# Optimization experiments

Measured on AMD Instinct MI355X. Metric: run time of the kernel, lower is better.

## Reference

```python
import jax, jax.numpy as jnp
import numpy as np

N_NODES = 100000
N_EDGES = 3200000
D_FEAT = 256
FILTERS = 256


def setup_inputs() -> dict:
    key = jax.random.key(0)
    k1, k2, k3, k4, k5 = jax.random.split(key, 5)
    x = jax.random.normal(k1, (N_NODES, D_FEAT), dtype=jnp.float32)
    edge_row = jax.random.randint(k2, (N_EDGES,), 0, N_NODES, dtype=jnp.int32)
    edge_col = jax.random.randint(k3, (N_EDGES,), 0, N_NODES, dtype=jnp.int32)
    edge_vals = jnp.ones((N_EDGES,), dtype=jnp.float32)
    w = jax.random.normal(k4, (D_FEAT, FILTERS), dtype=jnp.float32) * (2.0 / D_FEAT) ** 0.5  # he_normal
    b = jax.random.normal(k5, (FILTERS,), dtype=jnp.float32) * 0.05
    return {"x": x, "edge_row": edge_row, "edge_col": edge_col,
            "edge_vals": edge_vals, "w": w, "b": b}


def reference(x, edge_row, edge_col, edge_vals, w, b):
    n = x.shape[0]
    # normalize_A: D = rowsum(A); L = D^{-1/2} A D^{-1/2}
    deg = jax.ops.segment_sum(edge_vals, edge_row, num_segments=n)
    dinv = jnp.where(deg > 0, deg ** -0.5, 0.0)  # [N]
    norm_vals = edge_vals * dinv[edge_row] * dinv[edge_col]  # [E]
    # dense projection then sparse aggregation + bias + relu
    h = x @ w  # [N, F]
    msg = norm_vals[:, None] * h[edge_col]  # [E, F] gather + scale
    agg = jax.ops.segment_sum(msg, edge_row, num_segments=n)  # [N, F]
    return jax.nn.relu(agg + b)
```

## Files before the change

### kernel.cpp

```cpp
#include <hip/hip_runtime.h>
#include <hip/hip_bf16.h>


#define DF 256

typedef __attribute__((ext_vector_type(8))) short short8;
typedef __attribute__((ext_vector_type(4))) float f32x4;

__device__ __forceinline__ unsigned short f2bf(float f) {
    unsigned int u = __float_as_uint(f);
    unsigned int r = (u + 0x7fffu + ((u >> 16) & 1u)) >> 16;
    return (unsigned short)r;
}
__device__ __forceinline__ unsigned int pack2(float a, float b) {
    return (unsigned)f2bf(a) | ((unsigned)f2bf(b) << 16);
}
__device__ __forceinline__ float bflo(unsigned int u) { return __uint_as_float(u << 16); }
__device__ __forceinline__ float bfhi(unsigned int u) { return __uint_as_float(u & 0xffff0000u); }

__global__ void hist_rank_kernel(const int* __restrict__ row, int* __restrict__ cnt,
                                 int* __restrict__ rank, int E) {
    int e = blockIdx.x * blockDim.x + threadIdx.x;
    if (e < E) rank[e] = atomicAdd(&cnt[row[e]], 1);
}

__global__ __launch_bounds__(256) void scan1_kernel(const int* __restrict__ cnt,
                                                    int* __restrict__ bsum, int N) {
    __shared__ int red[256];
    int t = threadIdx.x;
    int base = blockIdx.x * 1024 + t * 4;
    int s = 0;
    if (base + 3 < N) {
        int4 v = *(const int4*)(cnt + base);
        s = v.x + v.y + v.z + v.w;
    } else {
        for (int k = 0; k < 4; ++k) if (base + k < N) s += cnt[base + k];
    }
    red[t] = s;
    __syncthreads();
    for (int off = 128; off > 0; off >>= 1) {
        if (t < off) red[t] += red[t + off];
        __syncthreads();
    }
    if (t == 0) bsum[blockIdx.x] = red[0];
}

__global__ __launch_bounds__(256) void scan2_kernel(const int* __restrict__ bsum,
                                                    int* __restrict__ bpre,
                                                    int* __restrict__ row_start, int B, int N) {
    __shared__ int ps[256];
    int t = threadIdx.x;
    int v = (t < B) ? bsum[t] : 0;
    ps[t] = v;
    __syncthreads();
    for (int off = 1; off < 256; off <<= 1) {
        int u = (t >= off) ? ps[t - off] : 0;
        __syncthreads();
        ps[t] += u;
        __syncthreads();
    }
    if (t < B) bpre[t] = ps[t] - v;
    if (t == 255) row_start[N] = ps[255];
}

__global__ __launch_bounds__(256) void scan3_kernel(const int* __restrict__ cnt,
                                                    const int* __restrict__ bpre,
                                                    int* __restrict__ row_start, int N) {
    __shared__ int ps[256];
    int t = threadIdx.x;
    int base = blockIdx.x * 1024 + t * 4;
    int v0 = 0, v1 = 0, v2 = 0, v3 = 0;
    if (base + 3 < N) {
        int4 v = *(const int4*)(cnt + base);
        v0 = v.x; v1 = v.y; v2 = v.z; v3 = v.w;
    } else {
        if (base < N) v0 = cnt[base];
        if (base + 1 < N) v1 = cnt[base + 1];
        if (base + 2 < N) v2 = cnt[base + 2];
        if (base + 3 < N) v3 = cnt[base + 3];
    }
    int tsum = v0 + v1 + v2 + v3;
    ps[t] = tsum;
    __syncthreads();
    for (int off = 1; off < 256; off <<= 1) {
        int u = (t >= off) ? ps[t - off] : 0;
        __syncthreads();
        ps[t] += u;
        __syncthreads();
    }
    int pre = bpre[blockIdx.x] + ps[t] - tsum;
    if (base < N) row_start[base] = pre;
    if (base + 1 < N) row_start[base + 1] = pre + v0;
    if (base + 2 < N) row_start[base + 2] = pre + v0 + v1;
    if (base + 3 < N) row_start[base + 3] = pre + v0 + v1 + v2;
}

__global__ void scatter_kernel(const int* __restrict__ row, const int* __restrict__ col,
                               const float* __restrict__ vals, const int* __restrict__ row_start,
                               const int* __restrict__ rank, int2* __restrict__ scv, int E) {
    int e = blockIdx.x * blockDim.x + threadIdx.x;
    if (e < E) {
        int r = row[e];
        int p = row_start[r] + rank[e];
        scv[p] = make_int2(col[e], __float_as_int(vals[e]));
    }
}

__global__ void degsum_kernel(const int2* __restrict__ scv, const int* __restrict__ row_start,
                              float* __restrict__ dinv, int N) {
    int r = blockIdx.x * blockDim.x + threadIdx.x;
    if (r < N) {
        int s = row_start[r], e = row_start[r + 1];
        float d = 0.f;
        for (int i = s; i < e; ++i) d += __int_as_float(scv[i].y);
        dinv[r] = (d > 0.f) ? (1.0f / sqrtf(d)) : 0.f;
    }
}

__global__ __launch_bounds__(256) void transpose_kernel(const float* __restrict__ w,
                                                        float* __restrict__ wT) {
    __shared__ float tile[32][33];
    int bx = blockIdx.x * 32, by = blockIdx.y * 32;
    int tx = threadIdx.x, ty = threadIdx.y;
    for (int j = ty; j < 32; j += 8) tile[j][tx] = w[(by + j) * DF + bx + tx];
    __syncthreads();
    for (int j = ty; j < 32; j += 8) wT[(bx + j) * DF + by + tx] = tile[tx][j];
}

__global__ __launch_bounds__(256) void gemm_kernel(const float* __restrict__ x,
                                                   const float* __restrict__ wT,
                                                   const float* __restrict__ dinv,
                                                   unsigned short* __restrict__ h, int N) {
    __shared__ unsigned short Al[128 * 32];
    __shared__ unsigned short Bl[128 * 32];
    int tid = threadIdx.x;
    int by = blockIdx.x, bx = blockIdx.y;
    int wv = tid >> 6, lane = tid & 63;
    int wr = wv >> 1, wc = wv & 1;
    int q = lane >> 4, mi = lane & 15;

    f32x4 acc[4][4];
#pragma unroll
    for (int i = 0; i < 4; ++i)
#pragma unroll
        for (int j = 0; j < 4; ++j) acc[i][j] = (f32x4){0.f, 0.f, 0.f, 0.f};

    int srow = tid >> 1;
    int sseg = (tid & 1) * 16;
    int axrow = by * 128 + srow; if (axrow >= N) axrow = N - 1;
    const float* ax = x + (long)axrow * DF + sseg;
    const float* bxp = wT + (long)(bx * 128 + srow) * DF + sseg;
    unsigned short* Aw = &Al[srow * 32 + sseg];
    unsigned short* Bw = &Bl[srow * 32 + sseg];

    for (int kk = 0; kk < DF; kk += 32) {
        float4 a0 = *(const float4*)(ax + kk);
        float4 a1 = *(const float4*)(ax + kk + 4);
        float4 a2 = *(const float4*)(ax + kk + 8);
        float4 a3 = *(const float4*)(ax + kk + 12);
        float4 b0 = *(const float4*)(bxp + kk);
        float4 b1 = *(const float4*)(bxp + kk + 4);
        float4 b2 = *(const float4*)(bxp + kk + 8);
        float4 b3 = *(const float4*)(bxp + kk + 12);
        __syncthreads();
        uint4 pa, pb;
        pa.x = pack2(a0.x, a0.y); pa.y = pack2(a0.z, a0.w);
        pa.z = pack2(a1.x, a1.y); pa.w = pack2(a1.z, a1.w);
        *(uint4*)Aw = pa;
        pa.x = pack2(a2.x, a2.y); pa.y = pack2(a2.z, a2.w);
        pa.z = pack2(a3.x, a3.y); pa.w = pack2(a3.z, a3.w);
        *(uint4*)(Aw + 8) = pa;
        pb.x = pack2(b0.x, b0.y); pb.y = pack2(b0.z, b0.w);
        pb.z = pack2(b1.x, b1.y); pb.w = pack2(b1.z, b1.w);
        *(uint4*)Bw = pb;
        pb.x = pack2(b2.x, b2.y); pb.y = pack2(b2.z, b2.w);
        pb.z = pack2(b3.x, b3.y); pb.w = pack2(b3.z, b3.w);
        *(uint4*)(Bw + 8) = pb;
        __syncthreads();

        short8 af[4], bf[4];
#pragma unroll
        for (int i = 0; i < 4; ++i)
            af[i] = *(const short8*)&Al[(wr * 64 + i * 16 + mi) * 32 + q * 8];
#pragma unroll
        for (int j = 0; j < 4; ++j)
            bf[j] = *(const short8*)&Bl[(wc * 64 + j * 16 + mi) * 32 + q * 8];
#pragma unroll
        for (int i = 0; i < 4; ++i)
#pragma unroll
            for (int j = 0; j < 4; ++j)
                acc[i][j] = __builtin_amdgcn_mfma_f32_16x16x32_bf16(af[i], bf[j], acc[i][j], 0, 0, 0);
    }

#pragma unroll
    for (int i = 0; i < 4; ++i) {
        int base_row = by * 128 + wr * 64 + i * 16 + q * 4;
#pragma unroll
        for (int r = 0; r < 4; ++r) {
            int rg = base_row + r;
            if (rg < N) {
                float dv = dinv[rg];
#pragma unroll
                for (int j = 0; j < 4; ++j) {
                    int cg = bx * 128 + wc * 64 + j * 16 + mi;
                    h[(long)rg * DF + cg] = f2bf(dv * acc[i][j][r]);
                }
            }
        }
    }
}

__global__ __launch_bounds__(256) void agg_kernel(const unsigned short* __restrict__ h,
                                                  const int* __restrict__ row_start,
                                                  const int2* __restrict__ scv,
                                                  const float* __restrict__ dinv,
                                                  const float* __restrict__ bias,
                                                  float* __restrict__ out, int N) {
    int wave = threadIdx.x >> 6;
    int lane = threadIdx.x & 63;
    int r = blockIdx.x * 4 + wave;
    if (r >= N) return;
    int half = lane >> 5;
    int fl = (lane & 31) * 8;
    int s = row_start[r], e = row_start[r + 1];
    float a0 = 0, a1 = 0, a2 = 0, a3 = 0, a4 = 0, a5 = 0, a6 = 0, a7 = 0;
    const unsigned short* hp = h + fl;
    int i = s + half;
    for (; i + 6 < e; i += 8) {
        int2 e0 = scv[i], e1 = scv[i + 2], e2 = scv[i + 4], e3 = scv[i + 6];
        uint4 u0 = *(const uint4*)(hp + (long)e0.x * DF);
        uint4 u1 = *(const uint4*)(hp + (long)e1.x * DF);
        uint4 u2 = *(const uint4*)(hp + (long)e2.x * DF);
        uint4 u3 = *(const uint4*)(hp + (long)e3.x * DF);
        float v0 = __int_as_float(e0.y), v1 = __int_as_float(e1.y);
        float v2 = __int_as_float(e2.y), v3 = __int_as_float(e3.y);
        a0 += v0 * bflo(u0.x) + v1 * bflo(u1.x) + v2 * bflo(u2.x) + v3 * bflo(u3.x);
        a1 += v0 * bfhi(u0.x) + v1 * bfhi(u1.x) + v2 * bfhi(u2.x) + v3 * bfhi(u3.x);
        a2 += v0 * bflo(u0.y) + v1 * bflo(u1.y) + v2 * bflo(u2.y) + v3 * bflo(u3.y);
        a3 += v0 * bfhi(u0.y) + v1 * bfhi(u1.y) + v2 * bfhi(u2.y) + v3 * bfhi(u3.y);
        a4 += v0 * bflo(u0.z) + v1 * bflo(u1.z) + v2 * bflo(u2.z) + v3 * bflo(u3.z);
        a5 += v0 * bfhi(u0.z) + v1 * bfhi(u1.z) + v2 * bfhi(u2.z) + v3 * bfhi(u3.z);
        a6 += v0 * bflo(u0.w) + v1 * bflo(u1.w) + v2 * bflo(u2.w) + v3 * bflo(u3.w);
        a7 += v0 * bfhi(u0.w) + v1 * bfhi(u1.w) + v2 * bfhi(u2.w) + v3 * bfhi(u3.w);
    }
    for (; i < e; i += 2) {
        int2 e0 = scv[i];
        float v0 = __int_as_float(e0.y);
        uint4 u0 = *(const uint4*)(hp + (long)e0.x * DF);
        a0 += v0 * bflo(u0.x); a1 += v0 * bfhi(u0.x);
        a2 += v0 * bflo(u0.y); a3 += v0 * bfhi(u0.y);
        a4 += v0 * bflo(u0.z); a5 += v0 * bfhi(u0.z);
        a6 += v0 * bflo(u0.w); a7 += v0 * bfhi(u0.w);
    }
    a0 += __shfl_xor(a0, 32); a1 += __shfl_xor(a1, 32);
    a2 += __shfl_xor(a2, 32); a3 += __shfl_xor(a3, 32);
    a4 += __shfl_xor(a4, 32); a5 += __shfl_xor(a5, 32);
    a6 += __shfl_xor(a6, 32); a7 += __shfl_xor(a7, 32);
    if (half == 0) {
        float dr = dinv[r];
        float4 b0 = *(const float4*)(bias + fl);
        float4 b1 = *(const float4*)(bias + fl + 4);
        float4 o0, o1;
        o0.x = fmaxf(fmaf(dr, a0, b0.x), 0.f);
        o0.y = fmaxf(fmaf(dr, a1, b0.y), 0.f);
        o0.z = fmaxf(fmaf(dr, a2, b0.z), 0.f);
        o0.w = fmaxf(fmaf(dr, a3, b0.w), 0.f);
        o1.x = fmaxf(fmaf(dr, a4, b1.x), 0.f);
        o1.y = fmaxf(fmaf(dr, a5, b1.y), 0.f);
        o1.z = fmaxf(fmaf(dr, a6, b1.z), 0.f);
        o1.w = fmaxf(fmaf(dr, a7, b1.w), 0.f);
        *(float4*)(out + (long)r * DF + fl) = o0;
        *(float4*)(out + (long)r * DF + fl + 4) = o1;
    }
}

extern "C" void kernel_launch(void* const* d_in, const int* in_sizes, int n_in,
                              void* d_out, int out_size, void* d_ws, size_t ws_size,
                              hipStream_t stream) {
    const float* x   = (const float*)d_in[0];
    const int* erow  = (const int*)d_in[1];
    const int* ecol  = (const int*)d_in[2];
    const float* ev  = (const float*)d_in[3];
    const float* w   = (const float*)d_in[4];
    const float* b   = (const float*)d_in[5];
    float* out = (float*)d_out;

    int N = in_sizes[0] / DF;
    int E = in_sizes[1];

    char* ws = (char*)d_ws;
    size_t Na  = (((size_t)N * 4) + 255) & ~(size_t)255;
    size_t RSa = (((size_t)(N + 1) * 4) + 255) & ~(size_t)255;
    size_t Ea  = (((size_t)E * 4) + 255) & ~(size_t)255;

    int*   cnt    = (int*)  (ws);
    float* wT     = (float*)(ws);
    float* dinv   = (float*)(ws + Na);
    int*   rstart = (int*)  (ws + 2 * Na);
    int2*  scv    = (int2*) (ws + 2 * Na + RSa);
    char*  un     = ws + 2 * Na + RSa + 2 * Ea;
    int*   rank   = (int*)un;
    unsigned short* h = (unsigned short*)un;
    int*   bsum   = (int*)(un + 16000000);
    int*   bpre   = (int*)(un + 16000000 + 4096);

    int B1 = (N + 1023) / 1024;

    hipMemsetAsync(cnt, 0, Na, stream);

    hist_rank_kernel<<<(E + 255) / 256, 256, 0, stream>>>(erow, cnt, rank, E);
    scan1_kernel<<<B1, 256, 0, stream>>>(cnt, bsum, N);
    scan2_kernel<<<1, 256, 0, stream>>>(bsum, bpre, rstart, B1, N);
    scan3_kernel<<<B1, 256, 0, stream>>>(cnt, bpre, rstart, N);
    scatter_kernel<<<(E + 255) / 256, 256, 0, stream>>>(erow, ecol, ev, rstart, rank, scv, E);
    degsum_kernel<<<(N + 255) / 256, 256, 0, stream>>>(scv, rstart, dinv, N);
    transpose_kernel<<<dim3(8, 8), dim3(32, 8), 0, stream>>>(w, wT);
    gemm_kernel<<<dim3((N + 127) / 128, DF / 128), 256, 0, stream>>>(x, wT, dinv, h, N);
    agg_kernel<<<(N + 3) / 4, 256, 0, stream>>>(h, rstart, scv, dinv, b, out, N);
}
```

Baseline: 692.2 us.

## Privatize row histogram per XCC to use workgroup-scope atomics

The edge-row histogram now keeps eight separate count arrays, one per XCC, indexed by the hardware XCC id, and uses relaxed workgroup-scope atomics that can resolve in the local L2 instead of device-scope atomics. Each edge's rank is packed with its XCC id, the scan sums the eight copies, and it writes a per-XCC base offset that the scatter uses to place edges. This aims to cut the cost of cross-die atomics in the histogram, at the price of an eight-times-larger memset, more scan traffic and a nondeterministic edge order within each row. Correctness relies on each XCC's L2 being coherent for its own atomics, so the workgroup-scope choice is a risk.

```diff
diff --git a/kernel.cpp b/kernel.cpp
--- a/kernel.cpp
+++ b/kernel.cpp
@@ -18,23 +18,39 @@
 __device__ __forceinline__ float bflo(unsigned int u) { return __uint_as_float(u << 16); }
 __device__ __forceinline__ float bfhi(unsigned int u) { return __uint_as_float(u & 0xffff0000u); }
 
-__global__ void hist_rank_kernel(const int* __restrict__ row, int* __restrict__ cnt,
-                                 int* __restrict__ rank, int E) {
+__device__ __forceinline__ unsigned xcc_id() {
+    unsigned x;
+    asm volatile("s_getreg_b32 %0, hwreg(HW_REG_XCC_ID)" : "=s"(x));
+    return x & 7u;
+}
+
+__global__ void hist_rank_kernel(const int* __restrict__ row, int* __restrict__ cntx,
+                                 int* __restrict__ rank, int Np, int E) {
     int e = blockIdx.x * blockDim.x + threadIdx.x;
-    if (e < E) rank[e] = atomicAdd(&cnt[row[e]], 1);
-}
-
-__global__ __launch_bounds__(256) void scan1_kernel(const int* __restrict__ cnt,
-                                                    int* __restrict__ bsum, int N) {
+    if (e < E) {
+        unsigned x = xcc_id();
+        int r = row[e];
+        int lr = __hip_atomic_fetch_add(&cntx[(size_t)x * Np + r], 1,
+                                        __ATOMIC_RELAXED, __HIP_MEMORY_SCOPE_WORKGROUP);
+        rank[e] = lr | (int)(x << 27);
+    }
+}
+
+__global__ __launch_bounds__(256) void scan1_kernel(const int* __restrict__ cntx,
+                                                    int* __restrict__ bsum, int Np, int N) {
     __shared__ int red[256];
     int t = threadIdx.x;
     int base = blockIdx.x * 1024 + t * 4;
     int s = 0;
     if (base + 3 < N) {
-        int4 v = *(const int4*)(cnt + base);
-        s = v.x + v.y + v.z + v.w;
+        for (int x = 0; x < 8; ++x) {
+            int4 v = *(const int4*)(cntx + (size_t)x * Np + base);
+            s += v.x + v.y + v.z + v.w;
+        }
     } else {
-        for (int k = 0; k < 4; ++k) if (base + k < N) s += cnt[base + k];
+        for (int x = 0; x < 8; ++x)
+            for (int k = 0; k < 4; ++k)
+                if (base + k < N) s += cntx[(size_t)x * Np + base + k];
     }
     red[t] = s;
     __syncthreads();
@@ -63,23 +79,31 @@
     if (t == 255) row_start[N] = ps[255];
 }
 
-__global__ __launch_bounds__(256) void scan3_kernel(const int* __restrict__ cnt,
+__global__ __launch_bounds__(256) void scan3_kernel(const int* __restrict__ cntx,
                                                     const int* __restrict__ bpre,
-                                                    int* __restrict__ row_start, int N) {
+                                                    int* __restrict__ row_start,
+                                                    int* __restrict__ basex, int Np, int N) {
     __shared__ int ps[256];
     int t = threadIdx.x;
     int base = blockIdx.x * 1024 + t * 4;
-    int v0 = 0, v1 = 0, v2 = 0, v3 = 0;
+    int v[8][4];
     if (base + 3 < N) {
-        int4 v = *(const int4*)(cnt + base);
-        v0 = v.x; v1 = v.y; v2 = v.z; v3 = v.w;
+        for (int x = 0; x < 8; ++x) {
+            int4 q = *(const int4*)(cntx + (size_t)x * Np + base);
+            v[x][0] = q.x; v[x][1] = q.y; v[x][2] = q.z; v[x][3] = q.w;
+        }
     } else {
-        if (base < N) v0 = cnt[base];
-        if (base + 1 < N) v1 = cnt[base + 1];
-        if (base + 2 < N) v2 = cnt[base + 2];
-        if (base + 3 < N) v3 = cnt[base + 3];
-    }
-    int tsum = v0 + v1 + v2 + v3;
+        for (int x = 0; x < 8; ++x)
+            for (int k = 0; k < 4; ++k)
+                v[x][k] = (base + k < N) ? cntx[(size_t)x * Np + base + k] : 0;
+    }
+    int tot[4];
+    for (int k = 0; k < 4; ++k) {
+        int s = 0;
+        for (int x = 0; x < 8; ++x) s += v[x][k];
+        tot[k] = s;
+    }
+    int tsum = tot[0] + tot[1] + tot[2] + tot[3];
     ps[t] = tsum;
     __syncthreads();
     for (int off = 1; off < 256; off <<= 1) {
@@ -89,19 +113,38 @@
         __syncthreads();
     }
     int pre = bpre[blockIdx.x] + ps[t] - tsum;
-    if (base < N) row_start[base] = pre;
-    if (base + 1 < N) row_start[base + 1] = pre + v0;
-    if (base + 2 < N) row_start[base + 2] = pre + v0 + v1;
-    if (base + 3 < N) row_start[base + 3] = pre + v0 + v1 + v2;
+    int acc[4];
+    acc[0] = pre;
+    acc[1] = acc[0] + tot[0];
+    acc[2] = acc[1] + tot[1];
+    acc[3] = acc[2] + tot[2];
+    if (base + 3 < N) {
+        *(int4*)(row_start + base) = make_int4(acc[0], acc[1], acc[2], acc[3]);
+        for (int x = 0; x < 8; ++x) {
+            *(int4*)(basex + (size_t)x * Np + base) = make_int4(acc[0], acc[1], acc[2], acc[3]);
+            for (int k = 0; k < 4; ++k) acc[k] += v[x][k];
+        }
+    } else {
+        for (int k = 0; k < 4; ++k) if (base + k < N) row_start[base + k] = acc[k];
+        for (int x = 0; x < 8; ++x)
+            for (int k = 0; k < 4; ++k) {
+                if (base + k < N) basex[(size_t)x * Np + base + k] = acc[k];
+                acc[k] += v[x][k];
+            }
+    }
 }
 
 __global__ void scatter_kernel(const int* __restrict__ row, const int* __restrict__ col,
-                               const float* __restrict__ vals, const int* __restrict__ row_start,
-                               const int* __restrict__ rank, int2* __restrict__ scv, int E) {
+                               const float* __restrict__ vals, const int* __restrict__ basex,
+                               const int* __restrict__ rank, int2* __restrict__ scv,
+                               int Np, int E) {
     int e = blockIdx.x * blockDim.x + threadIdx.x;
     if (e < E) {
         int r = row[e];
-        int p = row_start[r] + rank[e];
+        int pk = rank[e];
+        int x = ((unsigned)pk) >> 27;
+        int lr = pk & 0x07FFFFFF;
+        int p = basex[(size_t)x * Np + r] + lr;
         scv[p] = make_int2(col[e], __float_as_int(vals[e]));
     }
 }
@@ -292,27 +335,29 @@
     size_t Na  = (((size_t)N * 4) + 255) & ~(size_t)255;
     size_t RSa = (((size_t)(N + 1) * 4) + 255) & ~(size_t)255;
     size_t Ea  = (((size_t)E * 4) + 255) & ~(size_t)255;
-
-    int*   cnt    = (int*)  (ws);
+    int Np = (int)(Na >> 2);
+
     float* wT     = (float*)(ws);
     float* dinv   = (float*)(ws + Na);
     int*   rstart = (int*)  (ws + 2 * Na);
     int2*  scv    = (int2*) (ws + 2 * Na + RSa);
+    int*   cntx   = (int*)  (ws + 2 * Na + RSa);
     char*  un     = ws + 2 * Na + RSa + 2 * Ea;
     int*   rank   = (int*)un;
     unsigned short* h = (unsigned short*)un;
     int*   bsum   = (int*)(un + 16000000);
     int*   bpre   = (int*)(un + 16000000 + 4096);
+    int*   basex  = (int*)(un + 17000000);
 
     int B1 = (N + 1023) / 1024;
 
-    hipMemsetAsync(cnt, 0, Na, stream);
-
-    hist_rank_kernel<<<(E + 255) / 256, 256, 0, stream>>>(erow, cnt, rank, E);
-    scan1_kernel<<<B1, 256, 0, stream>>>(cnt, bsum, N);
+    hipMemsetAsync(cntx, 0, 8 * Na, stream);
+
+    hist_rank_kernel<<<(E + 255) / 256, 256, 0, stream>>>(erow, cntx, rank, Np, E);
+    scan1_kernel<<<B1, 256, 0, stream>>>(cntx, bsum, Np, N);
     scan2_kernel<<<1, 256, 0, stream>>>(bsum, bpre, rstart, B1, N);
-    scan3_kernel<<<B1, 256, 0, stream>>>(cnt, bpre, rstart, N);
-    scatter_kernel<<<(E + 255) / 256, 256, 0, stream>>>(erow, ecol, ev, rstart, rank, scv, E);
+    scan3_kernel<<<B1, 256, 0, stream>>>(cntx, bpre, rstart, basex, Np, N);
+    scatter_kernel<<<(E + 255) / 256, 256, 0, stream>>>(erow, ecol, ev, basex, rank, scv, Np, E);
     degsum_kernel<<<(N + 255) / 256, 256, 0, stream>>>(scv, rstart, dinv, N);
     transpose_kernel<<<dim3(8, 8), dim3(32, 8), 0, stream>>>(w, wT);
     gemm_kernel<<<dim3((N + 127) / 128, DF / 128), 256, 0, stream>>>(x, wT, dinv, h, N);
```

Result: no change. 691.0 us (-0.2%).

## Replace per-row CSR build with bucketed radix partition and in-block row sort

Applied to the files above, without the earlier changes.

Replaces the global-atomic histogram, three-pass scan and random scatter with a coarse bucket partition: per-chunk shared-memory histograms over 128-row buckets, a column-wise scan, and a scatter using shared atomics. Degree and aggregation then work per bucket, and the aggregation kernel sorts the bucket's edges by row in LDS before doing the same gather-accumulate. This is meant to cut the cost of the global atomics and of the scattered writes during CSR construction. In exchange there are fewer, heavier aggregation blocks (one per 128 rows) with large LDS use, which lowers occupancy. Buckets larger than the LDS capacity fall back to a slow rescan of the overflow edges.

```diff
diff --git a/kernel.cpp b/kernel.cpp
--- a/kernel.cpp
+++ b/kernel.cpp
@@ -2,7 +2,11 @@
 #include <hip/hip_bf16.h>
 
 
-#define DF 256
+#define DF   256
+#define RSH  7
+#define RPB  128
+#define CAP  4800
+#define CHUNK 8192
 
 typedef __attribute__((ext_vector_type(8))) short short8;
 typedef __attribute__((ext_vector_type(4))) float f32x4;
@@ -18,102 +22,99 @@
 __device__ __forceinline__ float bflo(unsigned int u) { return __uint_as_float(u << 16); }
 __device__ __forceinline__ float bfhi(unsigned int u) { return __uint_as_float(u & 0xffff0000u); }
 
-__global__ void hist_rank_kernel(const int* __restrict__ row, int* __restrict__ cnt,
-                                 int* __restrict__ rank, int E) {
-    int e = blockIdx.x * blockDim.x + threadIdx.x;
-    if (e < E) rank[e] = atomicAdd(&cnt[row[e]], 1);
-}
-
-__global__ __launch_bounds__(256) void scan1_kernel(const int* __restrict__ cnt,
-                                                    int* __restrict__ bsum, int N) {
-    __shared__ int red[256];
+__global__ __launch_bounds__(256) void bhist_kernel(const int* __restrict__ row,
+                                                    int* __restrict__ blockhist, int NB, int E) {
+    __shared__ int hist[1024];
     int t = threadIdx.x;
-    int base = blockIdx.x * 1024 + t * 4;
-    int s = 0;
-    if (base + 3 < N) {
-        int4 v = *(const int4*)(cnt + base);
-        s = v.x + v.y + v.z + v.w;
-    } else {
-        for (int k = 0; k < 4; ++k) if (base + k < N) s += cnt[base + k];
-    }
-    red[t] = s;
-    __syncthreads();
-    for (int off = 128; off > 0; off >>= 1) {
-        if (t < off) red[t] += red[t + off];
-        __syncthreads();
-    }
-    if (t == 0) bsum[blockIdx.x] = red[0];
-}
-
-__global__ __launch_bounds__(256) void scan2_kernel(const int* __restrict__ bsum,
-                                                    int* __restrict__ bpre,
-                                                    int* __restrict__ row_start, int B, int N) {
+    for (int i = t; i < NB; i += 256) hist[i] = 0;
+    __syncthreads();
+    int base = blockIdx.x * CHUNK;
+    int end = base + CHUNK; if (end > E) end = E;
+    for (int i = base + t; i < end; i += 256)
+        atomicAdd(&hist[row[i] >> RSH], 1);
+    __syncthreads();
+    for (int i = t; i < NB; i += 256)
+        blockhist[(size_t)blockIdx.x * NB + i] = hist[i];
+}
+
+__global__ __launch_bounds__(256) void bscan_kernel(int* __restrict__ blockhist,
+                                                    int* __restrict__ buckettot, int NB, int NBLK) {
     __shared__ int ps[256];
+    int b = blockIdx.x, t = threadIdx.x;
+    int e0 = 2 * t, e1 = 2 * t + 1;
+    int v0 = (e0 < NBLK) ? blockhist[(size_t)e0 * NB + b] : 0;
+    int v1 = (e1 < NBLK) ? blockhist[(size_t)e1 * NB + b] : 0;
+    int tsum = v0 + v1;
+    ps[t] = tsum;
+    __syncthreads();
+    for (int off = 1; off < 256; off <<= 1) {
+        int v = (t >= off) ? ps[t - off] : 0;
+        __syncthreads();
+        ps[t] += v;
+        __syncthreads();
+    }
+    int pre = ps[t] - tsum;
+    if (e0 < NBLK) blockhist[(size_t)e0 * NB + b] = pre;
+    if (e1 < NBLK) blockhist[(size_t)e1 * NB + b] = pre + v0;
+    if (t == 255) buckettot[b] = ps[255];
+}
+
+__global__ __launch_bounds__(1024) void btot_kernel(const int* __restrict__ buckettot,
+                                                    int* __restrict__ bucket_base, int NB) {
+    __shared__ int ps[1024];
     int t = threadIdx.x;
-    int v = (t < B) ? bsum[t] : 0;
+    int v = (t < NB) ? buckettot[t] : 0;
     ps[t] = v;
     __syncthreads();
-    for (int off = 1; off < 256; off <<= 1) {
+    for (int off = 1; off < 1024; off <<= 1) {
         int u = (t >= off) ? ps[t - off] : 0;
         __syncthreads();
         ps[t] += u;
         __syncthreads();
     }
-    if (t < B) bpre[t] = ps[t] - v;
-    if (t == 255) row_start[N] = ps[255];
-}
-
-__global__ __launch_bounds__(256) void scan3_kernel(const int* __restrict__ cnt,
-                                                    const int* __restrict__ bpre,
-                                                    int* __restrict__ row_start, int N) {
-    __shared__ int ps[256];
-    int t = threadIdx.x;
-    int base = blockIdx.x * 1024 + t * 4;
-    int v0 = 0, v1 = 0, v2 = 0, v3 = 0;
-    if (base + 3 < N) {
-        int4 v = *(const int4*)(cnt + base);
-        v0 = v.x; v1 = v.y; v2 = v.z; v3 = v.w;
-    } else {
-        if (base < N) v0 = cnt[base];
-        if (base + 1 < N) v1 = cnt[base + 1];
-        if (base + 2 < N) v2 = cnt[base + 2];
-        if (base + 3 < N) v3 = cnt[base + 3];
-    }
-    int tsum = v0 + v1 + v2 + v3;
-    ps[t] = tsum;
-    __syncthreads();
-    for (int off = 1; off < 256; off <<= 1) {
-        int u = (t >= off) ? ps[t - off] : 0;
-        __syncthreads();
-        ps[t] += u;
-        __syncthreads();
-    }
-    int pre = bpre[blockIdx.x] + ps[t] - tsum;
-    if (base < N) row_start[base] = pre;
-    if (base + 1 < N) row_start[base + 1] = pre + v0;
-    if (base + 2 < N) row_start[base + 2] = pre + v0 + v1;
-    if (base + 3 < N) row_start[base + 3] = pre + v0 + v1 + v2;
-}
-
-__global__ void scatter_kernel(const int* __restrict__ row, const int* __restrict__ col,
-                               const float* __restrict__ vals, const int* __restrict__ row_start,
-                               const int* __restrict__ rank, int2* __restrict__ scv, int E) {
-    int e = blockIdx.x * blockDim.x + threadIdx.x;
-    if (e < E) {
-        int r = row[e];
-        int p = row_start[r] + rank[e];
-        scv[p] = make_int2(col[e], __float_as_int(vals[e]));
-    }
-}
-
-__global__ void degsum_kernel(const int2* __restrict__ scv, const int* __restrict__ row_start,
-                              float* __restrict__ dinv, int N) {
-    int r = blockIdx.x * blockDim.x + threadIdx.x;
-    if (r < N) {
-        int s = row_start[r], e = row_start[r + 1];
-        float d = 0.f;
-        for (int i = s; i < e; ++i) d += __int_as_float(scv[i].y);
-        dinv[r] = (d > 0.f) ? (1.0f / sqrtf(d)) : 0.f;
+    if (t < NB) bucket_base[t] = ps[t] - v;
+    if (t == 1023) bucket_base[NB] = ps[1023];
+}
+
+__global__ __launch_bounds__(256) void bscatter_kernel(const int* __restrict__ row,
+                                                       const int* __restrict__ col,
+                                                       const float* __restrict__ vals,
+                                                       const int* __restrict__ blockhist,
+                                                       const int* __restrict__ bucket_base,
+                                                       int2* __restrict__ bedge, int NB, int E) {
+    __shared__ int loff[1024];
+    int t = threadIdx.x, blk = blockIdx.x;
+    for (int i = t; i < NB; i += 256)
+        loff[i] = bucket_base[i] + blockhist[(size_t)blk * NB + i];
+    __syncthreads();
+    int base = blk * CHUNK;
+    int end = base + CHUNK; if (end > E) end = E;
+    for (int i = base + t; i < end; i += 256) {
+        int r = row[i];
+        int p = atomicAdd(&loff[r >> RSH], 1);
+        bedge[p] = make_int2(((r & (RPB - 1)) << 17) | col[i], __float_as_int(vals[i]));
+    }
+}
+
+__global__ __launch_bounds__(256) void deg_kernel(const int2* __restrict__ bedge,
+                                                  const int* __restrict__ bucket_base,
+                                                  float* __restrict__ dinv, int N) {
+    __shared__ float acc[RPB];
+    int b = blockIdx.x, t = threadIdx.x;
+    if (t < RPB) acc[t] = 0.f;
+    __syncthreads();
+    int s = bucket_base[b], e = bucket_base[b + 1];
+    for (int i = s + t; i < e; i += 256) {
+        int2 ed = bedge[i];
+        atomicAdd(&acc[ed.x >> 17], __int_as_float(ed.y));
+    }
+    __syncthreads();
+    if (t < RPB) {
+        int r = b * RPB + t;
+        if (r < N) {
+            float d = acc[t];
+            dinv[r] = (d > 0.f) ? (1.0f / sqrtf(d)) : 0.f;
+        }
     }
 }
 
@@ -210,67 +211,114 @@
     }
 }
 
-__global__ __launch_bounds__(256) void agg_kernel(const unsigned short* __restrict__ h,
-                                                  const int* __restrict__ row_start,
-                                                  const int2* __restrict__ scv,
-                                                  const float* __restrict__ dinv,
-                                                  const float* __restrict__ bias,
-                                                  float* __restrict__ out, int N) {
-    int wave = threadIdx.x >> 6;
-    int lane = threadIdx.x & 63;
-    int r = blockIdx.x * 4 + wave;
-    if (r >= N) return;
+__global__ __launch_bounds__(256) void aggb_kernel(const unsigned short* __restrict__ h,
+                                                   const int2* __restrict__ bedge,
+                                                   const int* __restrict__ bucket_base,
+                                                   const float* __restrict__ dinv,
+                                                   const float* __restrict__ bias,
+                                                   float* __restrict__ out, int N) {
+    __shared__ int2 ledge[CAP];
+    __shared__ int cnt[RPB];
+    __shared__ int lrs[RPB + 1];
+    __shared__ int lfill[RPB];
+    int b = blockIdx.x, t = threadIdx.x;
+    int s = bucket_base[b], e = bucket_base[b + 1];
+    int tot = e - s;
+    int cap_end = s + (tot < CAP ? tot : CAP);
+    if (t < RPB) { cnt[t] = 0; lfill[t] = 0; }
+    __syncthreads();
+    for (int i = s + t; i < cap_end; i += 256)
+        atomicAdd(&cnt[bedge[i].x >> 17], 1);
+    __syncthreads();
+    int myc = 0;
+    if (t < RPB) { myc = cnt[t]; lrs[t] = myc; }
+    __syncthreads();
+    for (int off = 1; off < RPB; off <<= 1) {
+        int v = (t < RPB && t >= off) ? lrs[t - off] : 0;
+        __syncthreads();
+        if (t < RPB) lrs[t] += v;
+        __syncthreads();
+    }
+    if (t < RPB) {
+        int iv = lrs[t];
+        lrs[t] = iv - myc;
+        if (t == RPB - 1) lrs[RPB] = iv;
+    }
+    __syncthreads();
+    for (int i = s + t; i < cap_end; i += 256) {
+        int2 ed = bedge[i];
+        int rl = ed.x >> 17;
+        int p = lrs[rl] + atomicAdd(&lfill[rl], 1);
+        ledge[p] = make_int2(ed.x & 0x1FFFF, ed.y);
+    }
+    __syncthreads();
+    int wv = t >> 6, lane = t & 63;
     int half = lane >> 5;
     int fl = (lane & 31) * 8;
-    int s = row_start[r], e = row_start[r + 1];
-    float a0 = 0, a1 = 0, a2 = 0, a3 = 0, a4 = 0, a5 = 0, a6 = 0, a7 = 0;
     const unsigned short* hp = h + fl;
-    int i = s + half;
-    for (; i + 6 < e; i += 8) {
-        int2 e0 = scv[i], e1 = scv[i + 2], e2 = scv[i + 4], e3 = scv[i + 6];
-        uint4 u0 = *(const uint4*)(hp + (long)e0.x * DF);
-        uint4 u1 = *(const uint4*)(hp + (long)e1.x * DF);
-        uint4 u2 = *(const uint4*)(hp + (long)e2.x * DF);
-        uint4 u3 = *(const uint4*)(hp + (long)e3.x * DF);
-        float v0 = __int_as_float(e0.y), v1 = __int_as_float(e1.y);
-        float v2 = __int_as_float(e2.y), v3 = __int_as_float(e3.y);
-        a0 += v0 * bflo(u0.x) + v1 * bflo(u1.x) + v2 * bflo(u2.x) + v3 * bflo(u3.x);
-        a1 += v0 * bfhi(u0.x) + v1 * bfhi(u1.x) + v2 * bfhi(u2.x) + v3 * bfhi(u3.x);
-        a2 += v0 * bflo(u0.y) + v1 * bflo(u1.y) + v2 * bflo(u2.y) + v3 * bflo(u3.y);
-        a3 += v0 * bfhi(u0.y) + v1 * bfhi(u1.y) + v2 * bfhi(u2.y) + v3 * bfhi(u3.y);
-        a4 += v0 * bflo(u0.z) + v1 * bflo(u1.z) + v2 * bflo(u2.z) + v3 * bflo(u3.z);
-        a5 += v0 * bfhi(u0.z) + v1 * bfhi(u1.z) + v2 * bfhi(u2.z) + v3 * bfhi(u3.z);
-        a6 += v0 * bflo(u0.w) + v1 * bflo(u1.w) + v2 * bflo(u2.w) + v3 * bflo(u3.w);
-        a7 += v0 * bfhi(u0.w) + v1 * bfhi(u1.w) + v2 * bfhi(u2.w) + v3 * bfhi(u3.w);
-    }
-    for (; i < e; i += 2) {
-        int2 e0 = scv[i];
-        float v0 = __int_as_float(e0.y);
-        uint4 u0 = *(const uint4*)(hp + (long)e0.x * DF);
-        a0 += v0 * bflo(u0.x); a1 += v0 * bfhi(u0.x);
-        a2 += v0 * bflo(u0.y); a3 += v0 * bfhi(u0.y);
-        a4 += v0 * bflo(u0.z); a5 += v0 * bfhi(u0.z);
-        a6 += v0 * bflo(u0.w); a7 += v0 * bfhi(u0.w);
-    }
-    a0 += __shfl_xor(a0, 32); a1 += __shfl_xor(a1, 32);
-    a2 += __shfl_xor(a2, 32); a3 += __shfl_xor(a3, 32);
-    a4 += __shfl_xor(a4, 32); a5 += __shfl_xor(a5, 32);
-    a6 += __shfl_xor(a6, 32); a7 += __shfl_xor(a7, 32);
-    if (half == 0) {
-        float dr = dinv[r];
-        float4 b0 = *(const float4*)(bias + fl);
-        float4 b1 = *(const float4*)(bias + fl + 4);
-        float4 o0, o1;
-        o0.x = fmaxf(fmaf(dr, a0, b0.x), 0.f);
-        o0.y = fmaxf(fmaf(dr, a1, b0.y), 0.f);
-        o0.z = fmaxf(fmaf(dr, a2, b0.z), 0.f);
-        o0.w = fmaxf(fmaf(dr, a3, b0.w), 0.f);
-        o1.x = fmaxf(fmaf(dr, a4, b1.x), 0.f);
-        o1.y = fmaxf(fmaf(dr, a5, b1.y), 0.f);
-        o1.z = fmaxf(fmaf(dr, a6, b1.z), 0.f);
-        o1.w = fmaxf(fmaf(dr, a7, b1.w), 0.f);
-        *(float4*)(out + (long)r * DF + fl) = o0;
-        *(float4*)(out + (long)r * DF + fl + 4) = o1;
+    for (int lr = wv; lr < RPB; lr += 4) {
+        int r = b * RPB + lr;
+        if (r >= N) break;
+        int rs = lrs[lr], re = lrs[lr + 1];
+        float a0 = 0, a1 = 0, a2 = 0, a3 = 0, a4 = 0, a5 = 0, a6 = 0, a7 = 0;
+        int i = rs + half;
+        for (; i + 6 < re; i += 8) {
+            int2 e0 = ledge[i], e1 = ledge[i + 2], e2 = ledge[i + 4], e3 = ledge[i + 6];
+            uint4 u0 = *(const uint4*)(hp + (long)e0.x * DF);
+            uint4 u1 = *(const uint4*)(hp + (long)e1.x * DF);
+            uint4 u2 = *(const uint4*)(hp + (long)e2.x * DF);
+            uint4 u3 = *(const uint4*)(hp + (long)e3.x * DF);
+            float v0 = __int_as_float(e0.y), v1 = __int_as_float(e1.y);
+            float v2 = __int_as_float(e2.y), v3 = __int_as_float(e3.y);
+            a0 += v0 * bflo(u0.x) + v1 * bflo(u1.x) + v2 * bflo(u2.x) + v3 * bflo(u3.x);
+            a1 += v0 * bfhi(u0.x) + v1 * bfhi(u1.x) + v2 * bfhi(u2.x) + v3 * bfhi(u3.x);
+            a2 += v0 * bflo(u0.y) + v1 * bflo(u1.y) + v2 * bflo(u2.y) + v3 * bflo(u3.y);
+            a3 += v0 * bfhi(u0.y) + v1 * bfhi(u1.y) + v2 * bfhi(u2.y) + v3 * bfhi(u3.y);
+            a4 += v0 * bflo(u0.z) + v1 * bflo(u1.z) + v2 * bflo(u2.z) + v3 * bflo(u3.z);
+            a5 += v0 * bfhi(u0.z) + v1 * bfhi(u1.z) + v2 * bfhi(u2.z) + v3 * bfhi(u3.z);
+            a6 += v0 * bflo(u0.w) + v1 * bflo(u1.w) + v2 * bflo(u2.w) + v3 * bflo(u3.w);
+            a7 += v0 * bfhi(u0.w) + v1 * bfhi(u1.w) + v2 * bfhi(u2.w) + v3 * bfhi(u3.w);
+        }
+        for (; i < re; i += 2) {
+            int2 e0 = ledge[i];
+            float v0 = __int_as_float(e0.y);
+            uint4 u0 = *(const uint4*)(hp + (long)e0.x * DF);
+            a0 += v0 * bflo(u0.x); a1 += v0 * bfhi(u0.x);
+            a2 += v0 * bflo(u0.y); a3 += v0 * bfhi(u0.y);
+            a4 += v0 * bflo(u0.z); a5 += v0 * bfhi(u0.z);
+            a6 += v0 * bflo(u0.w); a7 += v0 * bfhi(u0.w);
+        }
+        for (int j = cap_end + half; j < e; j += 2) {
+            int2 ed = bedge[j];
+            if ((ed.x >> 17) == lr) {
+                float v0 = __int_as_float(ed.y);
+                uint4 u0 = *(const uint4*)(hp + (long)(ed.x & 0x1FFFF) * DF);
+                a0 += v0 * bflo(u0.x); a1 += v0 * bfhi(u0.x);
+                a2 += v0 * bflo(u0.y); a3 += v0 * bfhi(u0.y);
+                a4 += v0 * bflo(u0.z); a5 += v0 * bfhi(u0.z);
+                a6 += v0 * bflo(u0.w); a7 += v0 * bfhi(u0.w);
+            }
+        }
+        a0 += __shfl_xor(a0, 32); a1 += __shfl_xor(a1, 32);
+        a2 += __shfl_xor(a2, 32); a3 += __shfl_xor(a3, 32);
+        a4 += __shfl_xor(a4, 32); a5 += __shfl_xor(a5, 32);
+        a6 += __shfl_xor(a6, 32); a7 += __shfl_xor(a7, 32);
+        if (half == 0) {
+            float dr = dinv[r];
+            float4 b0 = *(const float4*)(bias + fl);
+            float4 b1 = *(const float4*)(bias + fl + 4);
+            float4 o0, o1;
+            o0.x = fmaxf(fmaf(dr, a0, b0.x), 0.f);
+            o0.y = fmaxf(fmaf(dr, a1, b0.y), 0.f);
+            o0.z = fmaxf(fmaf(dr, a2, b0.z), 0.f);
+            o0.w = fmaxf(fmaf(dr, a3, b0.w), 0.f);
+            o1.x = fmaxf(fmaf(dr, a4, b1.x), 0.f);
+            o1.y = fmaxf(fmaf(dr, a5, b1.y), 0.f);
+            o1.z = fmaxf(fmaf(dr, a6, b1.z), 0.f);
+            o1.w = fmaxf(fmaf(dr, a7, b1.w), 0.f);
+            *(float4*)(out + (long)r * DF + fl) = o0;
+            *(float4*)(out + (long)r * DF + fl + 4) = o1;
+        }
     }
 }
 
@@ -287,34 +335,30 @@
 
     int N = in_sizes[0] / DF;
     int E = in_sizes[1];
+    int NB = (N + RPB - 1) >> RSH;
+    int NBLK = (E + CHUNK - 1) / CHUNK;
 
     char* ws = (char*)d_ws;
+    size_t Ea8 = (((size_t)E * 8) + 255) & ~(size_t)255;
+    size_t Hs  = (((size_t)N * DF * 2) + 255) & ~(size_t)255;
     size_t Na  = (((size_t)N * 4) + 255) & ~(size_t)255;
-    size_t RSa = (((size_t)(N + 1) * 4) + 255) & ~(size_t)255;
-    size_t Ea  = (((size_t)E * 4) + 255) & ~(size_t)255;
-
-    int*   cnt    = (int*)  (ws);
-    float* wT     = (float*)(ws);
-    float* dinv   = (float*)(ws + Na);
-    int*   rstart = (int*)  (ws + 2 * Na);
-    int2*  scv    = (int2*) (ws + 2 * Na + RSa);
-    char*  un     = ws + 2 * Na + RSa + 2 * Ea;
-    int*   rank   = (int*)un;
-    unsigned short* h = (unsigned short*)un;
-    int*   bsum   = (int*)(un + 16000000);
-    int*   bpre   = (int*)(un + 16000000 + 4096);
-
-    int B1 = (N + 1023) / 1024;
-
-    hipMemsetAsync(cnt, 0, Na, stream);
-
-    hist_rank_kernel<<<(E + 255) / 256, 256, 0, stream>>>(erow, cnt, rank, E);
-    scan1_kernel<<<B1, 256, 0, stream>>>(cnt, bsum, N);
-    scan2_kernel<<<1, 256, 0, stream>>>(bsum, bpre, rstart, B1, N);
-    scan3_kernel<<<B1, 256, 0, stream>>>(cnt, bpre, rstart, N);
-    scatter_kernel<<<(E + 255) / 256, 256, 0, stream>>>(erow, ecol, ev, rstart, rank, scv, E);
-    degsum_kernel<<<(N + 255) / 256, 256, 0, stream>>>(scv, rstart, dinv, N);
+
+    int2* bedge = (int2*)ws;
+    char* reg2 = ws + Ea8;
+    unsigned short* h = (unsigned short*)reg2;
+    int* blockhist = (int*)reg2;
+    char* reg3 = reg2 + Hs;
+    float* wT = (float*)reg3;
+    float* dinv = (float*)(reg3 + 262144);
+    int* buckettot = (int*)(reg3 + 262144 + Na);
+    int* bucket_base = (int*)(reg3 + 262144 + Na + 8192);
+
+    bhist_kernel<<<NBLK, 256, 0, stream>>>(erow, blockhist, NB, E);
+    bscan_kernel<<<NB, 256, 0, stream>>>(blockhist, buckettot, NB, NBLK);
+    btot_kernel<<<1, 1024, 0, stream>>>(buckettot, bucket_base, NB);
+    bscatter_kernel<<<NBLK, 256, 0, stream>>>(erow, ecol, ev, blockhist, bucket_base, bedge, NB, E);
+    deg_kernel<<<NB, 256, 0, stream>>>(bedge, bucket_base, dinv, N);
     transpose_kernel<<<dim3(8, 8), dim3(32, 8), 0, stream>>>(w, wT);
     gemm_kernel<<<dim3((N + 127) / 128, DF / 128), 256, 0, stream>>>(x, wT, dinv, h, N);
-    agg_kernel<<<(N + 3) / 4, 256, 0, stream>>>(h, rstart, scv, dinv, b, out, N);
-}
+    aggb_kernel<<<NB, 256, 0, stream>>>(h, bedge, bucket_base, dinv, b, out, N);
+}
```

Measured after the change: 595.9 us. 1.16x faster.
